# Performance work log

Measured on AMD Instinct MI355X. Metric: run time of the kernel, lower is better.

## Reference

```python
import jax, jax.numpy as jnp
import numpy as np

B, L, E = 8, 2048, 4096
TOKEN_DIM, EDGE_DIM, HIDDEN = 768, 256, 128


def setup_inputs() -> dict:
    key = jax.random.key(0)
    k1, k2, k3, k4, k5 = jax.random.split(key, 5)
    token_embedding = jax.random.normal(k1, (B, L, TOKEN_DIM), dtype=jnp.float32)
    edge_embedding = jax.random.normal(k2, (B, E, EDGE_DIM), dtype=jnp.float32)
    # fc: Linear(token_dim+edge_dim -> hidden, bias=False); stored as [in, out]
    W_fc = jax.random.normal(k3, (TOKEN_DIM + EDGE_DIM, HIDDEN), dtype=jnp.float32) * 0.02
    # attn_fc: Linear(2*hidden -> 1); weight flattened to [2*hidden], plus scalar bias
    a_attn = jax.random.normal(k4, (2 * HIDDEN,), dtype=jnp.float32) * 0.02
    b_attn = jax.random.normal(k5, (1,), dtype=jnp.float32) * 0.02
    return {"token_embedding": token_embedding, "edge_embedding": edge_embedding,
            "W_fc": W_fc, "a_attn": a_attn, "b_attn": b_attn}


def reference(token_embedding, edge_embedding, W_fc, a_attn, b_attn):
    # avg edge embedding, broadcast over sequence
    avg_edge = edge_embedding.mean(axis=1, keepdims=True)          # [B, 1, De]
    avg_edge = jnp.broadcast_to(avg_edge, (token_embedding.shape[0],
                                           token_embedding.shape[1],
                                           avg_edge.shape[-1]))     # [B, L, De]
    combined = jnp.concatenate([token_embedding, avg_edge], axis=-1)  # [B, L, Dt+De]
    h = jnp.einsum('bld,dh->blh', combined, W_fc)                   # [B, L, H]

    # Additive attention decomposition: a^T [h_j || h_i] = a1.h_j + a2.h_i
    # (original builds concat([h_repeat_row (=h_j), h_repeat_col (=h_i)]))
    H = h.shape[-1]
    a1, a2 = a_attn[:H], a_attn[H:]
    s_j = jnp.einsum('blh,h->bl', h, a1)                            # score contrib from h_j
    s_i = jnp.einsum('blh,h->bl', h, a2)                            # score contrib from h_i
    scores = s_i[:, :, None] + s_j[:, None, :] + b_attn[0]          # [B, L, L], scores[b,i,j]
    attn = jax.nn.softmax(scores, axis=-1)                          # softmax over j
    h_prime = jnp.einsum('bij,bjh->bih', attn, h)                   # [B, L, H]
    return h_prime
```

## Files before the change

kernel.cpp:

```cpp
#include <hip/hip_runtime.h>

constexpr int Bn  = 8;
constexpr int Ln  = 2048;
constexpr int En  = 4096;
constexpr int TDn = 768;
constexpr int EDn = 256;
constexpr int Hn  = 128;

constexpr int OFF_V1    = 0;
constexpr int OFF_DEN   = 768;
constexpr int OFF_T     = 1024;
constexpr int OFF_ES    = 8192;
constexpr int OFF_ROW   = 10240;
constexpr int OFF_EPART = 16384;
constexpr int OFF_TPART = 278528;
constexpr int REC = 772;

__global__ __launch_bounds__(256)
void K0(const float* __restrict__ edge, const float* __restrict__ W,
        const float* __restrict__ a, float* __restrict__ ws) {
    const int tid = threadIdx.x, wv = tid >> 6, lane = tid & 63;
    __shared__ float4 s_red[4][64];

    if (blockIdx.x < 192) {
        int d = blockIdx.x * 4 + wv;
        float acc = W[d * Hn + lane]      * a[lane]
                  + W[d * Hn + 64 + lane] * a[64 + lane];
        #pragma unroll
        for (int off = 32; off > 0; off >>= 1)
            acc += __shfl_down(acc, off, 64);
        if (lane == 0) ws[OFF_V1 + d] = acc;
        return;
    }
    int eb = blockIdx.x - 192;
    int b = eb >> 7, chunk = eb & 127;
    const float4* e4 = (const float4*)edge
                     + ((size_t)(b * En + chunk * 32 + wv * 8)) * (EDn / 4) + lane;
    float4 acc = {0.f, 0.f, 0.f, 0.f};
    #pragma unroll
    for (int i = 0; i < 8; ++i) {
        float4 v = e4[(size_t)i * (EDn / 4)];
        acc.x += v.x; acc.y += v.y; acc.z += v.z; acc.w += v.w;
    }
    s_red[wv][lane] = acc;
    __syncthreads();
    if (tid < 64) {
        float4 r0 = s_red[0][tid], r1 = s_red[1][tid],
               r2 = s_red[2][tid], r3 = s_red[3][tid];
        float4 s = {r0.x + r1.x + r2.x + r3.x, r0.y + r1.y + r2.y + r3.y,
                    r0.z + r1.z + r2.z + r3.z, r0.w + r1.w + r2.w + r3.w};
        ((float4*)(ws + OFF_EPART))[eb * 64 + tid] = s;
    }
}

__global__ __launch_bounds__(256)
void K1(const float* __restrict__ token, float* __restrict__ ws) {
    __shared__ float4 s_v1[TDn / 4];
    __shared__ float  s_s[16];
    __shared__ float  s_e[16];
    const int tid = threadIdx.x, wv = tid >> 6, lane = tid & 63;
    const int b = blockIdx.x >> 7, chunk = blockIdx.x & 127;
    const size_t row0 = (size_t)(b * Ln + chunk * 16);

    if (tid < TDn / 4) s_v1[tid] = ((const float4*)(ws + OFF_V1))[tid];
    __syncthreads();

    #pragma unroll
    for (int i = 0; i < 4; ++i) {
        int li = wv * 4 + i;
        const float4* t4 = (const float4*)token + (row0 + li) * (TDn / 4);
        float acc = 0.f;
        #pragma unroll
        for (int j = 0; j < 3; ++j) {
            float4 t = t4[lane + 64 * j];
            float4 v = s_v1[lane + 64 * j];
            acc += t.x * v.x + t.y * v.y + t.z * v.z + t.w * v.w;
        }
        #pragma unroll
        for (int off = 32; off > 0; off >>= 1)
            acc += __shfl_down(acc, off, 64);
        if (lane == 0) s_s[li] = acc;
    }
    __syncthreads();

    if (tid < 16) s_e[tid] = expf(s_s[tid]);
    __syncthreads();

    float sum = 0.f;
    #pragma unroll
    for (int l = 0; l < 16; ++l) sum += s_e[l];

    const float* tok = token + row0 * TDn;
    float a0 = 0.f, a1 = 0.f, a2 = 0.f;
    #pragma unroll 4
    for (int l = 0; l < 16; ++l) {
        float e = s_e[l];
        const float* r = tok + (size_t)l * TDn;
        a0 += e * r[tid];
        a1 += e * r[tid + 256];
        a2 += e * r[tid + 512];
    }
    float* rec = ws + OFF_TPART + (size_t)blockIdx.x * REC;
    if (tid == 0) rec[0] = sum;
    rec[4 + tid]       = a0;
    rec[4 + tid + 256] = a1;
    rec[4 + tid + 512] = a2;
}

__global__ __launch_bounds__(256)
void K2(float* __restrict__ ws) {
    const int tid = threadIdx.x;
    if (blockIdx.x < 24) {
        int b = blockIdx.x >> 2;
        int part = blockIdx.x - (blockIdx.x / 3) * 3;
        b = blockIdx.x / 3;
        const float* recs = ws + OFF_TPART + (size_t)(b * 128) * REC + 4 + part * 256;
        float acc = 0.f;
        #pragma unroll 4
        for (int k = 0; k < 128; ++k) acc += recs[(size_t)k * REC + tid];
        ws[OFF_T + b * TDn + part * 256 + tid] = acc;
    } else {
        int b = blockIdx.x - 24;
        const float* p = ws + OFF_EPART + (size_t)(b * 128) * EDn + tid;
        float acc = 0.f;
        #pragma unroll 4
        for (int k = 0; k < 128; ++k) acc += p[(size_t)k * EDn];
        ws[OFF_ES + b * EDn + tid] = acc * (1.0f / En);

        __shared__ float s_red[128];
        if (tid < 128) {
            s_red[tid] = ws[OFF_TPART + (size_t)(b * 128 + tid) * REC];
        }
        __syncthreads();
        if (tid < 64)  { s_red[tid] += s_red[tid + 64]; } __syncthreads();
        if (tid < 32)  { s_red[tid] += s_red[tid + 32]; } __syncthreads();
        if (tid < 16)  { s_red[tid] += s_red[tid + 16]; } __syncthreads();
        if (tid == 0) {
            float d = 0.f;
            #pragma unroll
            for (int i = 0; i < 16; ++i) d += s_red[i];
            ws[OFF_DEN + b] = d;
        }
    }
}

__global__ __launch_bounds__(1024)
void K3(const float* __restrict__ W, float* __restrict__ ws) {
    __shared__ float s_c[1024];
    __shared__ float s_red[1024];
    const int b = blockIdx.x, tid = threadIdx.x;
    float invden = 1.0f / ws[OFF_DEN + b];
    s_c[tid] = (tid < TDn) ? ws[OFF_T + b * TDn + tid] * invden
                           : ws[OFF_ES + b * EDn + (tid - TDn)];
    __syncthreads();

    int h = tid & 127, dg = tid >> 7;
    const float* w = W + (dg * 128) * Hn + h;
    float acc = 0.f;
    #pragma unroll 4
    for (int i = 0; i < 128; ++i)
        acc += s_c[dg * 128 + i] * w[i * Hn];
    s_red[tid] = acc;
    __syncthreads();
    if (tid < 128) {
        float r = 0.f;
        #pragma unroll
        for (int g = 0; g < 8; ++g) r += s_red[g * 128 + tid];
        ws[OFF_ROW + b * Hn + tid] = r;
    }
}

__global__ __launch_bounds__(256)
void K4(const float* __restrict__ ws, float4* __restrict__ out) {
    int idx = blockIdx.x * blockDim.x + threadIdx.x;
    int b = idx >> 16;
    int q = idx & (Hn / 4 - 1);
    out[idx] = ((const float4*)(ws + OFF_ROW))[b * (Hn / 4) + q];
}

extern "C" void kernel_launch(void* const* d_in, const int* in_sizes, int n_in,
                              void* d_out, int out_size, void* d_ws, size_t ws_size,
                              hipStream_t stream) {
    const float* token = (const float*)d_in[0];
    const float* edge  = (const float*)d_in[1];
    const float* W     = (const float*)d_in[2];
    const float* a     = (const float*)d_in[3];
    float* ws  = (float*)d_ws;
    float4* out = (float4*)d_out;

    K0 <<<1216, 256,  0, stream>>>(edge, W, a, ws);
    K1 <<<1024, 256,  0, stream>>>(token, ws);
    K2 <<<32,   256,  0, stream>>>(ws);
    K3 <<<Bn,   1024, 0, stream>>>(W, ws);
    K4 <<<2048, 256,  0, stream>>>(ws, out);
}
```

Measured before the change: 144.2 us.

## Merge edge reduction with token pass and widen final projection grid

```diff
diff --git a/kernel.cpp b/kernel.cpp
--- a/kernel.cpp
+++ b/kernel.cpp
@@ -17,49 +17,52 @@
 constexpr int REC = 772;
 
 __global__ __launch_bounds__(256)
-void K0(const float* __restrict__ edge, const float* __restrict__ W,
-        const float* __restrict__ a, float* __restrict__ ws) {
+void K_init(const float* __restrict__ W, const float* __restrict__ a,
+            float* __restrict__ ws) {
+    const int tid = threadIdx.x, wv = tid >> 6, lane = tid & 63;
+    int d = blockIdx.x * 4 + wv;
+    float acc = W[d * Hn + lane]      * a[lane]
+              + W[d * Hn + 64 + lane] * a[64 + lane];
+    #pragma unroll
+    for (int off = 32; off > 0; off >>= 1)
+        acc += __shfl_down(acc, off, 64);
+    if (lane == 0) ws[OFF_V1 + d] = acc;
+}
+
+__global__ __launch_bounds__(256)
+void K_main(const float* __restrict__ token, const float* __restrict__ edge,
+            float* __restrict__ ws) {
     const int tid = threadIdx.x, wv = tid >> 6, lane = tid & 63;
     __shared__ float4 s_red[4][64];
-
-    if (blockIdx.x < 192) {
-        int d = blockIdx.x * 4 + wv;
-        float acc = W[d * Hn + lane]      * a[lane]
-                  + W[d * Hn + 64 + lane] * a[64 + lane];
-        #pragma unroll
-        for (int off = 32; off > 0; off >>= 1)
-            acc += __shfl_down(acc, off, 64);
-        if (lane == 0) ws[OFF_V1 + d] = acc;
-        return;
-    }
-    int eb = blockIdx.x - 192;
-    int b = eb >> 7, chunk = eb & 127;
-    const float4* e4 = (const float4*)edge
-                     + ((size_t)(b * En + chunk * 32 + wv * 8)) * (EDn / 4) + lane;
-    float4 acc = {0.f, 0.f, 0.f, 0.f};
-    #pragma unroll
-    for (int i = 0; i < 8; ++i) {
-        float4 v = e4[(size_t)i * (EDn / 4)];
-        acc.x += v.x; acc.y += v.y; acc.z += v.z; acc.w += v.w;
-    }
-    s_red[wv][lane] = acc;
-    __syncthreads();
-    if (tid < 64) {
-        float4 r0 = s_red[0][tid], r1 = s_red[1][tid],
-               r2 = s_red[2][tid], r3 = s_red[3][tid];
-        float4 s = {r0.x + r1.x + r2.x + r3.x, r0.y + r1.y + r2.y + r3.y,
-                    r0.z + r1.z + r2.z + r3.z, r0.w + r1.w + r2.w + r3.w};
-        ((float4*)(ws + OFF_EPART))[eb * 64 + tid] = s;
-    }
-}
-
-__global__ __launch_bounds__(256)
-void K1(const float* __restrict__ token, float* __restrict__ ws) {
     __shared__ float4 s_v1[TDn / 4];
     __shared__ float  s_s[16];
     __shared__ float  s_e[16];
-    const int tid = threadIdx.x, wv = tid >> 6, lane = tid & 63;
-    const int b = blockIdx.x >> 7, chunk = blockIdx.x & 127;
+
+    if (blockIdx.x < 1024) {
+        int eb = blockIdx.x;
+        int b = eb >> 7, chunk = eb & 127;
+        const float4* e4 = (const float4*)edge
+                         + ((size_t)(b * En + chunk * 32 + wv * 8)) * (EDn / 4) + lane;
+        float4 acc = {0.f, 0.f, 0.f, 0.f};
+        #pragma unroll
+        for (int i = 0; i < 8; ++i) {
+            float4 v = e4[(size_t)i * (EDn / 4)];
+            acc.x += v.x; acc.y += v.y; acc.z += v.z; acc.w += v.w;
+        }
+        s_red[wv][lane] = acc;
+        __syncthreads();
+        if (tid < 64) {
+            float4 r0 = s_red[0][tid], r1 = s_red[1][tid],
+                   r2 = s_red[2][tid], r3 = s_red[3][tid];
+            float4 s = {r0.x + r1.x + r2.x + r3.x, r0.y + r1.y + r2.y + r3.y,
+                        r0.z + r1.z + r2.z + r3.z, r0.w + r1.w + r2.w + r3.w};
+            ((float4*)(ws + OFF_EPART))[eb * 64 + tid] = s;
+        }
+        return;
+    }
+
+    int tb = blockIdx.x - 1024;
+    const int b = tb >> 7, chunk = tb & 127;
     const size_t row0 = (size_t)(b * Ln + chunk * 16);
 
     if (tid < TDn / 4) s_v1[tid] = ((const float4*)(ws + OFF_V1))[tid];
@@ -100,7 +103,7 @@
         a1 += e * r[tid + 256];
         a2 += e * r[tid + 512];
     }
-    float* rec = ws + OFF_TPART + (size_t)blockIdx.x * REC;
+    float* rec = ws + OFF_TPART + (size_t)tb * REC;
     if (tid == 0) rec[0] = sum;
     rec[4 + tid]       = a0;
     rec[4 + tid + 256] = a1;
@@ -111,9 +114,7 @@
 void K2(float* __restrict__ ws) {
     const int tid = threadIdx.x;
     if (blockIdx.x < 24) {
-        int b = blockIdx.x >> 2;
-        int part = blockIdx.x - (blockIdx.x / 3) * 3;
-        b = blockIdx.x / 3;
+        int b = blockIdx.x / 3, part = blockIdx.x % 3;
         const float* recs = ws + OFF_TPART + (size_t)(b * 128) * REC + 4 + part * 256;
         float acc = 0.f;
         #pragma unroll 4
@@ -128,9 +129,8 @@
         ws[OFF_ES + b * EDn + tid] = acc * (1.0f / En);
 
         __shared__ float s_red[128];
-        if (tid < 128) {
+        if (tid < 128)
             s_red[tid] = ws[OFF_TPART + (size_t)(b * 128 + tid) * REC];
-        }
         __syncthreads();
         if (tid < 64)  { s_red[tid] += s_red[tid + 64]; } __syncthreads();
         if (tid < 32)  { s_red[tid] += s_red[tid + 32]; } __syncthreads();
@@ -144,29 +144,36 @@
     }
 }
 
-__global__ __launch_bounds__(1024)
+__global__ __launch_bounds__(256)
 void K3(const float* __restrict__ W, float* __restrict__ ws) {
     __shared__ float s_c[1024];
-    __shared__ float s_red[1024];
-    const int b = blockIdx.x, tid = threadIdx.x;
+    __shared__ float s_red[256];
+    const int b = blockIdx.x >> 3, hg = blockIdx.x & 7;
+    const int tid = threadIdx.x;
+    const int hidx = tid & 15, dseg = tid >> 4;
+    const int h = hg * 16 + hidx;
+
     float invden = 1.0f / ws[OFF_DEN + b];
-    s_c[tid] = (tid < TDn) ? ws[OFF_T + b * TDn + tid] * invden
-                           : ws[OFF_ES + b * EDn + (tid - TDn)];
-    __syncthreads();
-
-    int h = tid & 127, dg = tid >> 7;
-    const float* w = W + (dg * 128) * Hn + h;
+    #pragma unroll
+    for (int k = 0; k < 4; ++k) {
+        int i = tid + k * 256;
+        s_c[i] = (i < TDn) ? ws[OFF_T + b * TDn + i] * invden
+                           : ws[OFF_ES + b * EDn + (i - TDn)];
+    }
+    __syncthreads();
+
+    const float* w = W + (dseg * 64) * Hn + h;
     float acc = 0.f;
     #pragma unroll 4
-    for (int i = 0; i < 128; ++i)
-        acc += s_c[dg * 128 + i] * w[i * Hn];
+    for (int i = 0; i < 64; ++i)
+        acc += s_c[dseg * 64 + i] * w[i * Hn];
     s_red[tid] = acc;
     __syncthreads();
-    if (tid < 128) {
+    if (tid < 16) {
         float r = 0.f;
         #pragma unroll
-        for (int g = 0; g < 8; ++g) r += s_red[g * 128 + tid];
-        ws[OFF_ROW + b * Hn + tid] = r;
+        for (int g = 0; g < 16; ++g) r += s_red[g * 16 + tid];
+        ws[OFF_ROW + b * Hn + hg * 16 + tid] = r;
     }
 }
 
@@ -188,9 +195,9 @@
     float* ws  = (float*)d_ws;
     float4* out = (float4*)d_out;
 
-    K0 <<<1216, 256,  0, stream>>>(edge, W, a, ws);
-    K1 <<<1024, 256,  0, stream>>>(token, ws);
-    K2 <<<32,   256,  0, stream>>>(ws);
-    K3 <<<Bn,   1024, 0, stream>>>(W, ws);
-    K4 <<<2048, 256,  0, stream>>>(ws, out);
-}
+    K_init<<<192,  256, 0, stream>>>(W, a, ws);
+    K_main<<<2048, 256, 0, stream>>>(token, edge, ws);
+    K2    <<<32,   256, 0, stream>>>(ws);
+    K3    <<<64,   256, 0, stream>>>(W, ws);
+    K4    <<<2048, 256, 0, stream>>>(ws, out);
+}
```

New measurement: 136.3 us. -5.5%, faster.
